# Performance work log

Hardware: AMD Instinct MI355X
Metric: run time of the kernel (lower is better)

Reference implementation:

```python
import jax, jax.numpy as jnp
import numpy as np

N_EMBD = 1024
N_HEAD = 16
HEAD_SIZE = N_EMBD // N_HEAD
EPS = 1e-5


def layernorm(x, g, b):
    mu = jnp.mean(x, axis=-1, keepdims=True)
    var = jnp.var(x, axis=-1, keepdims=True)
    return (x - mu) * jax.lax.rsqrt(var + EPS) * g + b


def setup_inputs() -> dict:
    key = jax.random.key(0)
    ks = jax.random.split(key, 12)
    s = 0.02
    C = N_EMBD
    return {
        "x": jax.random.normal(ks[0], (2, 2048, C), dtype=jnp.float32),
        "Wq": jax.random.normal(ks[1], (C, C), dtype=jnp.float32) * s,
        "Wk": jax.random.normal(ks[2], (C, C), dtype=jnp.float32) * s,
        "Wv": jax.random.normal(ks[3], (C, C), dtype=jnp.float32) * s,
        "Wo": jax.random.normal(ks[4], (C, C), dtype=jnp.float32) * s,
        "bo": jnp.zeros((C,), dtype=jnp.float32),
        "W1": jax.random.normal(ks[5], (C, 4 * C), dtype=jnp.float32) * s,
        "b1": jnp.zeros((4 * C,), dtype=jnp.float32),
        "W2": jax.random.normal(ks[6], (4 * C, C), dtype=jnp.float32) * s,
        "b2": jnp.zeros((C,), dtype=jnp.float32),
        "ln1_g": jnp.ones((C,), dtype=jnp.float32),
        "ln1_b": jnp.zeros((C,), dtype=jnp.float32),
        "ln2_g": jnp.ones((C,), dtype=jnp.float32),
        "ln2_b": jnp.zeros((C,), dtype=jnp.float32),
    }


def reference(x, Wq, Wk, Wv, Wo, bo, W1, b1, W2, b2, ln1_g, ln1_b, ln2_g, ln2_b):
    B, T, C = x.shape
    H, Dh = N_HEAD, HEAD_SIZE

    # --- self-attention branch ---
    h = layernorm(x, ln1_g, ln1_b)
    q = (h @ Wq).reshape(B, T, H, Dh)
    k = (h @ Wk).reshape(B, T, H, Dh)
    v = (h @ Wv).reshape(B, T, H, Dh)

    # NOTE: original scales by C**-0.5 (n_embd), not head_size**-0.5
    scale = C ** (-0.5)
    scores = jnp.einsum("bqhd,bkhd->bhqk", q, k) * scale  # [B,H,T,T]
    causal = jnp.tril(jnp.ones((T, T), dtype=bool))
    scores = jnp.where(causal, scores, -jnp.inf)
    wei = jax.nn.softmax(scores, axis=-1)
    attn = jnp.einsum("bhqk,bkhd->bqhd", wei, v).reshape(B, T, C)
    x = x + attn @ Wo + bo

    # --- MLP branch ---
    h2 = layernorm(x, ln2_g, ln2_b)
    ff = jax.nn.relu(h2 @ W1 + b1) @ W2 + b2
    return x + ff
```

## Files before the change

### kernel.cpp

```cpp
#include <hip/hip_runtime.h>

typedef unsigned short u16;
typedef __bf16 bf16;
typedef bf16 bf16x8 __attribute__((ext_vector_type(8)));
typedef float f32x4 __attribute__((ext_vector_type(4)));


__device__ __forceinline__ u16 f2bf(float f) {
  bf16 b = (bf16)f;
  return __builtin_bit_cast(u16, b);
}

__device__ __forceinline__ void gll16(void* lds, const void* g) {
  __builtin_amdgcn_global_load_lds((__attribute__((address_space(1))) void*)g,
                                   (__attribute__((address_space(3))) void*)lds,
                                   16, 0, 0);
}

__device__ __forceinline__ f32x4 mfma16(bf16x8 a, bf16x8 b, f32x4 c) {
  return __builtin_amdgcn_mfma_f32_16x16x32_bf16(a, b, c, 0, 0, 0);
}



__global__ __launch_bounds__(256)
void transpose_all(const float* __restrict__ Wq, const float* __restrict__ Wk,
                   const float* __restrict__ Wv, const float* __restrict__ Wo,
                   const float* __restrict__ W1, const float* __restrict__ W2,
                   u16* __restrict__ WqT, u16* __restrict__ WkT,
                   u16* __restrict__ WvT, u16* __restrict__ WoT,
                   u16* __restrict__ W1T, u16* __restrict__ W2T) {
  __shared__ float tile[32][33];
  const int id = blockIdx.x;
  const float* src;
  u16* dst;
  int R, C, t;
  if (id < 4096) {
    const int w = id >> 10;
    t = id & 1023; R = 1024; C = 1024;
    src = w == 0 ? Wq : w == 1 ? Wk : w == 2 ? Wv : Wo;
    dst = w == 0 ? WqT : w == 1 ? WkT : w == 2 ? WvT : WoT;
  } else if (id < 8192) {
    t = id - 4096; R = 1024; C = 4096; src = W1; dst = W1T;
  } else {
    t = id - 8192; R = 4096; C = 1024; src = W2; dst = W2T;
  }
  const int tilesx = C >> 5;
  const int c0 = (t % tilesx) * 32, r0 = (t / tilesx) * 32;
  const int tx = threadIdx.x, ty = threadIdx.y;
#pragma unroll
  for (int i = 0; i < 4; ++i)
    tile[ty + i * 8][tx] = src[(size_t)(r0 + ty + i * 8) * C + c0 + tx];
  __syncthreads();
#pragma unroll
  for (int i = 0; i < 4; ++i)
    dst[(size_t)(c0 + ty + i * 8) * R + r0 + tx] = f2bf(tile[tx][ty + i * 8]);
}


__global__ __launch_bounds__(256)
void ln_kernel(const float* __restrict__ x, const float* __restrict__ g,
               const float* __restrict__ bb, u16* __restrict__ h) {
  const int row = blockIdx.x;
  const int tid = threadIdx.x;
  const float4 xv = ((const float4*)(x + (size_t)row * 1024))[tid];
  float s = xv.x + xv.y + xv.z + xv.w;
  float q = xv.x * xv.x + xv.y * xv.y + xv.z * xv.z + xv.w * xv.w;
#pragma unroll
  for (int m = 1; m < 64; m <<= 1) {
    s += __shfl_xor(s, m);
    q += __shfl_xor(q, m);
  }
  __shared__ float ss[4], qq[4];
  const int wid = tid >> 6, lane = tid & 63;
  if (lane == 0) { ss[wid] = s; qq[wid] = q; }
  __syncthreads();
  s = ss[0] + ss[1] + ss[2] + ss[3];
  q = qq[0] + qq[1] + qq[2] + qq[3];
  const float mean = s * (1.0f / 1024.0f);
  const float var = q * (1.0f / 1024.0f) - mean * mean;
  const float rs = rsqrtf(var + 1e-5f);
  const float4 gv = ((const float4*)g)[tid];
  const float4 bv = ((const float4*)bb)[tid];
  ushort4 o;
  o.x = f2bf((xv.x - mean) * rs * gv.x + bv.x);
  o.y = f2bf((xv.y - mean) * rs * gv.y + bv.y);
  o.z = f2bf((xv.z - mean) * rs * gv.z + bv.z);
  o.w = f2bf((xv.w - mean) * rs * gv.w + bv.w);
  ((ushort4*)(h + (size_t)row * 1024))[tid] = o;
}


__device__ __forceinline__ void xcd_swizzle(int& bx, int& by, int& bz) {
  const int gx = gridDim.x, gy = gridDim.y;
  const int nwg = gx * gy * (int)gridDim.z;
  int flat = (int)blockIdx.x + gx * ((int)blockIdx.y + gy * (int)blockIdx.z);
  flat = (flat & 7) * (nwg >> 3) + (flat >> 3);
  bx = flat % gx;
  const int rem = flat / gx;
  by = rem % gy;
  bz = rem / gy;
}


template <int EPI>
__global__ __launch_bounds__(256)
void gemm_bt(const u16* __restrict__ A, const u16* __restrict__ Bt,
             const float* __restrict__ bias,
             void* __restrict__ O0, void* __restrict__ O1, void* __restrict__ O2,
             int M, int N, int K) {
  __shared__ __align__(16) u16 Alds[3][128 * 32];
  __shared__ __align__(16) u16 Blds[3][128 * 32];
  const int tid = threadIdx.x;
  const int lane = tid & 63, wid = tid >> 6;
  const int rl = lane & 15, kg = lane >> 4;
  const int ksw = (rl >> 1) & 3;
  int bx, by, bz;
  xcd_swizzle(bx, by, bz);
  const int m0 = by * 128, n0 = bx * 128;
  f32x4 acc[4][4];
#pragma unroll
  for (int i = 0; i < 4; ++i)
#pragma unroll
    for (int j = 0; j < 4; ++j) acc[i][j] = (f32x4){0.f, 0.f, 0.f, 0.f};
  const int wr = wid >> 1, wc = wid & 1;
  const int c0 = wid * 2, c1 = wid * 2 + 1;
  const int srow0 = c0 * 16 + (lane >> 2);
  const int srow1 = c1 * 16 + (lane >> 2);
  const int skol = (((lane & 3) ^ ((lane >> 3) & 3))) * 8;

#define STAGE_BT(buf, k0)                                                      \
  {                                                                            \
    gll16(Alds[buf] + c0 * 512, A + (size_t)(m0 + srow0) * K + (k0) + skol);   \
    gll16(Alds[buf] + c1 * 512, A + (size_t)(m0 + srow1) * K + (k0) + skol);   \
    gll16(Blds[buf] + c0 * 512, Bt + (size_t)(n0 + srow0) * K + (k0) + skol);  \
    gll16(Blds[buf] + c1 * 512, Bt + (size_t)(n0 + srow1) * K + (k0) + skol);  \
  }

  const int nt = K >> 5;
  STAGE_BT(0, 0);
  STAGE_BT(1, 32);
  int cur = 0;
  for (int t = 0; t < nt; ++t) {
    if (t + 1 < nt)
      asm volatile("s_waitcnt vmcnt(4)" ::: "memory");
    else
      asm volatile("s_waitcnt vmcnt(0)" ::: "memory");
    __builtin_amdgcn_s_barrier();
    if (t + 2 < nt) {
      const int nxt = cur >= 1 ? cur - 1 : cur + 2;
      STAGE_BT(nxt, (t + 2) << 5);
    }
    bf16x8 af[4], bfr[4];
#pragma unroll
    for (int m = 0; m < 4; ++m)
      af[m] = *(const bf16x8*)(Alds[cur] + (wr * 64 + m * 16 + rl) * 32 +
                               (kg ^ ksw) * 8);
#pragma unroll
    for (int n = 0; n < 4; ++n)
      bfr[n] = *(const bf16x8*)(Blds[cur] + (wc * 64 + n * 16 + rl) * 32 +
                                (kg ^ ksw) * 8);
    __builtin_amdgcn_s_setprio(1);
#pragma unroll
    for (int m = 0; m < 4; ++m)
#pragma unroll
      for (int n = 0; n < 4; ++n)
        acc[m][n] = mfma16(af[m], bfr[n], acc[m][n]);
    __builtin_amdgcn_s_setprio(0);
    cur = cur + 1 == 3 ? 0 : cur + 1;
  }
#undef STAGE_BT

#pragma unroll
  for (int m = 0; m < 4; ++m) {
#pragma unroll
    for (int n = 0; n < 4; ++n) {
      const int col = n0 + wc * 64 + n * 16 + rl;
      const int row0 = m0 + wr * 64 + m * 16 + kg * 4;
      if (EPI == 0) {
        const int seg = col >> 10;
        const int lc = col & 1023;
        if (seg == 2) {
          u16* vt = (u16*)O2;
          const size_t off =
              ((size_t)((row0 >> 11) * 16 + (lc >> 6)) * 64 + (lc & 63)) * 2048 +
              (row0 & 2047);
          ushort4 pk = {f2bf(acc[m][n][0]), f2bf(acc[m][n][1]),
                        f2bf(acc[m][n][2]), f2bf(acc[m][n][3])};
          *(ushort4*)(vt + off) = pk;
        } else {
          u16* o = (u16*)(seg == 0 ? O0 : O1);
#pragma unroll
          for (int r = 0; r < 4; ++r)
            o[(size_t)(row0 + r) * 1024 + lc] = f2bf(acc[m][n][r]);
        }
      } else {
        const float bv = bias[col];
#pragma unroll
        for (int r = 0; r < 4; ++r) {
          float v = acc[m][n][r] + bv;
          v = v > 0.f ? v : 0.f;
          ((u16*)O0)[(size_t)(row0 + r) * N + col] = f2bf(v);
        }
      }
    }
  }
}


__global__ __launch_bounds__(256)
void gemm64(const u16* __restrict__ A, const u16* __restrict__ Bt,
            const float* __restrict__ bias, const float* __restrict__ res,
            float* __restrict__ O, int M, int N, int K) {
  __shared__ __align__(16) u16 Alds[4][64 * 32];
  __shared__ __align__(16) u16 Blds[4][128 * 32];
  const int tid = threadIdx.x;
  const int lane = tid & 63, wid = tid >> 6;
  const int rl = lane & 15, kg = lane >> 4;
  const int ksw = (rl >> 1) & 3;
  int bx, by, bz;
  xcd_swizzle(bx, by, bz);
  const int m0 = by * 64, n0 = bx * 128;
  f32x4 acc[2][4];
#pragma unroll
  for (int i = 0; i < 2; ++i)
#pragma unroll
    for (int j = 0; j < 4; ++j) acc[i][j] = (f32x4){0.f, 0.f, 0.f, 0.f};
  const int wr = wid >> 1, wc = wid & 1;
  const int srow = lane >> 2;
  const int skol = (((lane & 3) ^ ((lane >> 3) & 3))) * 8;
  const int arow = wid * 16 + srow;
  const int brow0 = wid * 32 + srow;
  const int brow1 = wid * 32 + 16 + srow;

#define STAGE_64(buf, k0)                                                      \
  {                                                                            \
    gll16(Alds[buf] + wid * 512, A + (size_t)(m0 + arow) * K + (k0) + skol);   \
    gll16(Blds[buf] + wid * 1024,                                              \
          Bt + (size_t)(n0 + brow0) * K + (k0) + skol);                        \
    gll16(Blds[buf] + wid * 1024 + 512,                                        \
          Bt + (size_t)(n0 + brow1) * K + (k0) + skol);                        \
  }

  const int nt = K >> 5;
  STAGE_64(0, 0);
  STAGE_64(1, 32);
  STAGE_64(2, 64);
  for (int t = 0; t < nt; ++t) {
    const int cur = t & 3;
    if (t + 2 < nt)
      asm volatile("s_waitcnt vmcnt(6)" ::: "memory");
    else if (t + 1 < nt)
      asm volatile("s_waitcnt vmcnt(3)" ::: "memory");
    else
      asm volatile("s_waitcnt vmcnt(0)" ::: "memory");
    __builtin_amdgcn_s_barrier();
    if (t + 3 < nt) STAGE_64((t + 3) & 3, (t + 3) << 5);
    bf16x8 af[2], bfr[4];
#pragma unroll
    for (int m = 0; m < 2; ++m)
      af[m] = *(const bf16x8*)(Alds[cur] + (wr * 32 + m * 16 + rl) * 32 +
                               (kg ^ ksw) * 8);
#pragma unroll
    for (int n = 0; n < 4; ++n)
      bfr[n] = *(const bf16x8*)(Blds[cur] + (wc * 64 + n * 16 + rl) * 32 +
                                (kg ^ ksw) * 8);
    __builtin_amdgcn_s_setprio(1);
#pragma unroll
    for (int m = 0; m < 2; ++m)
#pragma unroll
      for (int n = 0; n < 4; ++n)
        acc[m][n] = mfma16(af[m], bfr[n], acc[m][n]);
    __builtin_amdgcn_s_setprio(0);
  }
#undef STAGE_64

#pragma unroll
  for (int m = 0; m < 2; ++m) {
#pragma unroll
    for (int n = 0; n < 4; ++n) {
      const int col = n0 + wc * 64 + n * 16 + rl;
      const int row0 = m0 + wr * 32 + m * 16 + kg * 4;
      const float bv = bias[col];
#pragma unroll
      for (int r = 0; r < 4; ++r) {
        const int row = row0 + r;
        O[(size_t)row * N + col] =
            acc[m][n][r] + bv + res[(size_t)row * N + col];
      }
    }
  }
}


#define SC2 0.045084220027780106f

__device__ __forceinline__ void attn_range(
    const u16* __restrict__ qg, const u16* __restrict__ kgl,
    const u16* __restrict__ vtb, size_t rowb, int cb, char* plw,
    int rl, int kg, int q0, int kvb, int kve, bool mask_last,
    f32x4 (&ot)[2][4], float (&lrun)[2]) {
  if (kvb >= kve) return;
  const int swz = (rl & 7) << 4;
  bf16x8 qf[2][2];
#pragma unroll
  for (int m = 0; m < 2; ++m) {
    const u16* qp = qg + (rowb + q0 + m * 16 + rl) * 1024 + cb + kg * 8;
    qf[m][0] = *(const bf16x8*)(qp);
    qf[m][1] = *(const bf16x8*)(qp + 32);
  }

  bf16x8 ka[4][2], kb[4][2];
#define LOADK(dst, kvi)                                                        \
  {                                                                            \
    const u16* krow = kgl + (rowb + (kvi) * 64 + rl) * 1024 + cb + kg * 8;     \
    _Pragma("unroll") for (int n = 0; n < 4; ++n) {                            \
      dst[n][0] = *(const bf16x8*)(krow + (size_t)n * 16 * 1024);              \
      dst[n][1] = *(const bf16x8*)(krow + (size_t)n * 16 * 1024 + 32);         \
    }                                                                          \
  }

#define BODY(kf, kvi)                                                          \
  {                                                                            \
    const int kv0 = (kvi) * 64;                                                \
    const u16* vrow = vtb + (size_t)rl * 2048 + kv0 + kg * 8;                  \
    bf16x8 vfr[4][2];                                                          \
    _Pragma("unroll") for (int dt = 0; dt < 4; ++dt) {                         \
      vfr[dt][0] = *(const bf16x8*)(vrow + (size_t)dt * 16 * 2048);            \
      vfr[dt][1] = *(const bf16x8*)(vrow + (size_t)dt * 16 * 2048 + 32);       \
    }                                                                          \
    const bool domask = mask_last && ((kvi) == kve - 1);                       \
    _Pragma("unroll") for (int m = 0; m < 2; ++m) {                            \
      f32x4 s[4];                                                              \
      __builtin_amdgcn_s_setprio(1);                                           \
      _Pragma("unroll") for (int n = 0; n < 4; ++n) {                          \
        f32x4 t = (f32x4){0.f, 0.f, 0.f, 0.f};                                 \
        t = mfma16(kf[n][0], qf[m][0], t);                                     \
        t = mfma16(kf[n][1], qf[m][1], t);                                     \
        s[n] = t;                                                              \
      }                                                                        \
      __builtin_amdgcn_s_setprio(0);                                           \
      if (domask) {                                                            \
        const int qrow = q0 + m * 16 + rl;                                     \
        _Pragma("unroll") for (int n = 0; n < 4; ++n)                          \
            _Pragma("unroll") for (int r = 0; r < 4; ++r) {                    \
          const int tk = kv0 + n * 16 + 4 * kg + r;                            \
          s[n][r] = (tk > qrow) ? -3e38f : s[n][r];                            \
        }                                                                      \
      }                                                                        \
      float ps = 0.f;                                                          \
      _Pragma("unroll") for (int n = 0; n < 4; ++n) {                          \
        const float p0 = exp2f(__builtin_fmaf(s[n][0], SC2, -8.f));            \
        const float p1 = exp2f(__builtin_fmaf(s[n][1], SC2, -8.f));            \
        const float p2 = exp2f(__builtin_fmaf(s[n][2], SC2, -8.f));            \
        const float p3 = exp2f(__builtin_fmaf(s[n][3], SC2, -8.f));            \
        ps += (p0 + p1) + (p2 + p3);                                           \
        ushort4 pk = {f2bf(p0), f2bf(p1), f2bf(p2), f2bf(p3)};                 \
        *(ushort4*)(plw + m * 2048 + ((rl * 128 + n * 32 + kg * 8) ^ swz)) =   \
            pk;                                                                \
      }                                                                        \
      lrun[m] += ps;                                                           \
    }                                                                          \
    _Pragma("unroll") for (int m = 0; m < 2; ++m) {                            \
      const bf16x8 pf0 =                                                       \
          *(const bf16x8*)(plw + m * 2048 + ((rl * 128 + kg * 16) ^ swz));     \
      const bf16x8 pf1 = *(const bf16x8*)(plw + m * 2048 +                     \
                                          ((rl * 128 + 64 + kg * 16) ^ swz));  \
      __builtin_amdgcn_s_setprio(1);                                           \
      _Pragma("unroll") for (int dt = 0; dt < 4; ++dt) {                       \
        ot[m][dt] = mfma16(vfr[dt][0], pf0, ot[m][dt]);                        \
        ot[m][dt] = mfma16(vfr[dt][1], pf1, ot[m][dt]);                        \
      }                                                                        \
      __builtin_amdgcn_s_setprio(0);                                           \
    }                                                                          \
  }

  LOADK(ka, kvb);
  int kv = kvb;
  for (;;) {
    if (kv + 1 < kve) LOADK(kb, kv + 1);
    BODY(ka, kv);
    ++kv;
    if (kv >= kve) break;
    if (kv + 1 < kve) LOADK(ka, kv + 1);
    BODY(kb, kv);
    ++kv;
    if (kv >= kve) break;
  }
#undef LOADK
#undef BODY
}

__global__ __launch_bounds__(128)
void attn_kernel(const u16* __restrict__ qg, const u16* __restrict__ kgl,
                 const u16* __restrict__ vtg, u16* __restrict__ og) {
  const int tid = threadIdx.x, lane = tid & 63, wid = tid >> 6;
  const int rl = lane & 15, kg = lane >> 4;
  const int flat = blockIdx.x;
  const int bh = (flat & 7) * 4 + ((flat >> 3) & 3);
  const int pr = flat >> 5;
  const int jA = pr, jB = 63 - pr;
  const int nA = (jA >> 1) + 1, nB = (jB >> 1) + 1;
  const int a = (nB - nA) >> 1;
  const size_t rowb = (size_t)(bh >> 4) * 2048;
  const int cb = (bh & 15) * 64;
  const u16* vtb = vtg + (size_t)bh * 64 * 2048;

  __shared__ __align__(16) char Pl[2][4096];
  __shared__ __align__(16) float MrgO[2][4][64][4];
  __shared__ float MrgL[2][16];
  char* plw = Pl[wid];

  f32x4 ot[2][4];
  float lrun[2] = {0.f, 0.f};
#pragma unroll
  for (int m = 0; m < 2; ++m)
#pragma unroll
    for (int dt = 0; dt < 4; ++dt) ot[m][dt] = (f32x4){0.f, 0.f, 0.f, 0.f};

  if (wid == 0) {
    attn_range(qg, kgl, vtb, rowb, cb, plw, rl, kg, jA * 32, 0, nA, true,
               ot, lrun);
#pragma unroll
    for (int m = 0; m < 2; ++m) {
      lrun[m] += __shfl_xor(lrun[m], 16);
      lrun[m] += __shfl_xor(lrun[m], 32);
      const float inv = 1.f / lrun[m];
      u16* orow = og + (rowb + jA * 32 + m * 16 + rl) * 1024 + cb;
#pragma unroll
      for (int dt = 0; dt < 4; ++dt) {
        ushort4 ok = {f2bf(ot[m][dt][0] * inv), f2bf(ot[m][dt][1] * inv),
                      f2bf(ot[m][dt][2] * inv), f2bf(ot[m][dt][3] * inv)};
        *(ushort4*)(orow + dt * 16 + 4 * kg) = ok;
      }
      lrun[m] = 0.f;
#pragma unroll
      for (int dt = 0; dt < 4; ++dt) ot[m][dt] = (f32x4){0.f, 0.f, 0.f, 0.f};
    }
    attn_range(qg, kgl, vtb, rowb, cb, plw, rl, kg, jB * 32, 0, a, false,
               ot, lrun);
  } else {
    attn_range(qg, kgl, vtb, rowb, cb, plw, rl, kg, jB * 32, a, nB, true,
               ot, lrun);
#pragma unroll
    for (int m = 0; m < 2; ++m) {
      lrun[m] += __shfl_xor(lrun[m], 16);
      lrun[m] += __shfl_xor(lrun[m], 32);
#pragma unroll
      for (int dt = 0; dt < 4; ++dt)
        *(f32x4*)(&MrgO[m][dt][lane][0]) = ot[m][dt];
      if (kg == 0) MrgL[m][rl] = lrun[m];
    }
  }
  __syncthreads();
  if (wid == 0) {
#pragma unroll
    for (int m = 0; m < 2; ++m) {
      lrun[m] += __shfl_xor(lrun[m], 16);
      lrun[m] += __shfl_xor(lrun[m], 32);
      const float inv = 1.f / (lrun[m] + MrgL[m][rl]);
      u16* orow = og + (rowb + jB * 32 + m * 16 + rl) * 1024 + cb;
#pragma unroll
      for (int dt = 0; dt < 4; ++dt) {
        const f32x4 o1 = *(const f32x4*)(&MrgO[m][dt][lane][0]);
        ushort4 ok;
#pragma unroll
        for (int r = 0; r < 4; ++r)
          ((u16*)&ok)[r] = f2bf((ot[m][dt][r] + o1[r]) * inv);
        *(ushort4*)(orow + dt * 16 + 4 * kg) = ok;
      }
    }
  }
}


extern "C" void kernel_launch(void* const* d_in, const int* in_sizes, int n_in,
                              void* d_out, int out_size, void* d_ws, size_t ws_size,
                              hipStream_t stream) {
  const float* x    = (const float*)d_in[0];
  const float* Wq   = (const float*)d_in[1];
  const float* Wk   = (const float*)d_in[2];
  const float* Wv   = (const float*)d_in[3];
  const float* Wo   = (const float*)d_in[4];
  const float* bo   = (const float*)d_in[5];
  const float* W1   = (const float*)d_in[6];
  const float* b1   = (const float*)d_in[7];
  const float* W2   = (const float*)d_in[8];
  const float* b2   = (const float*)d_in[9];
  const float* ln1g = (const float*)d_in[10];
  const float* ln1b = (const float*)d_in[11];
  const float* ln2g = (const float*)d_in[12];
  const float* ln2b = (const float*)d_in[13];
  float* out = (float*)d_out;

  char* ws = (char*)d_ws;
  const size_t MB = 1024 * 1024;
  u16* WqT  = (u16*)(ws + 0 * MB);
  u16* WoT  = (u16*)(ws + 6 * MB);
  u16* W1T  = (u16*)(ws + 8 * MB);
  u16* W2T  = (u16*)(ws + 16 * MB);
  u16* h    = (u16*)(ws + 24 * MB);
  u16* q    = (u16*)(ws + 32 * MB);
  u16* k    = (u16*)(ws + 40 * MB);
  u16* vt   = (u16*)(ws + 48 * MB);
  u16* attn = (u16*)(ws + 56 * MB);
  float* x1 = (float*)(ws + 64 * MB);
  u16* ff1  = (u16*)(ws + 32 * MB);
  u16* WkT  = WqT + 1024 * 1024;
  u16* WvT  = WqT + 2 * 1024 * 1024;

  dim3 tblk(32, 8);
  transpose_all<<<12288, tblk, 0, stream>>>(Wq, Wk, Wv, Wo, W1, W2,
                                            WqT, WkT, WvT, WoT, W1T, W2T);

  ln_kernel<<<4096, 256, 0, stream>>>(x, ln1g, ln1b, h);

  gemm_bt<0><<<dim3(24, 32), 256, 0, stream>>>(h, WqT, nullptr,
                                               q, k, vt, 4096, 3072, 1024);

  attn_kernel<<<1024, 128, 0, stream>>>(q, k, vt, attn);

  gemm64<<<dim3(8, 64), 256, 0, stream>>>(attn, WoT, bo, x, x1,
                                          4096, 1024, 1024);

  ln_kernel<<<4096, 256, 0, stream>>>(x1, ln2g, ln2b, h);

  gemm_bt<1><<<dim3(32, 32), 256, 0, stream>>>(h, W1T, b1, ff1, ff1, ff1,
                                               4096, 4096, 1024);

  gemm64<<<dim3(8, 64), 256, 0, stream>>>(ff1, W2T, b2, x1, out,
                                          4096, 1024, 4096);
}
```

Baseline: 269.7 us.

## Split attention KV range across four waves and widen gemm64 K-tile

The attention kernel now gives each block a single 32-row query tile and splits its causal KV range across four waves, merging the partial outputs and row sums through shared memory. This replaces the paired short/long tile balancing between two waves, doubling the block count for more parallelism. Separately, gemm64 moves from a K-step of 32 with four LDS buffers to a K-step of 64 with three buffers and an XOR swizzle over eight 16-byte slots, halving barriers per K. The risks are extra LDS for the partial merge, which may lower occupancy, and three-stage rather than four-stage buffering in the GEMM.

```diff
diff --git a/kernel.cpp b/kernel.cpp
--- a/kernel.cpp
+++ b/kernel.cpp
@@ -20,7 +20,6 @@
 __device__ __forceinline__ f32x4 mfma16(bf16x8 a, bf16x8 b, f32x4 c) {
   return __builtin_amdgcn_mfma_f32_16x16x32_bf16(a, b, c, 0, 0, 0);
 }
-
 
 
 __global__ __launch_bounds__(256)
@@ -212,12 +211,11 @@
 void gemm64(const u16* __restrict__ A, const u16* __restrict__ Bt,
             const float* __restrict__ bias, const float* __restrict__ res,
             float* __restrict__ O, int M, int N, int K) {
-  __shared__ __align__(16) u16 Alds[4][64 * 32];
-  __shared__ __align__(16) u16 Blds[4][128 * 32];
+  __shared__ __align__(16) u16 Alds[3][64 * 64];
+  __shared__ __align__(16) u16 Blds[3][128 * 64];
   const int tid = threadIdx.x;
   const int lane = tid & 63, wid = tid >> 6;
   const int rl = lane & 15, kg = lane >> 4;
-  const int ksw = (rl >> 1) & 3;
   int bx, by, bz;
   xcd_swizzle(bx, by, bz);
   const int m0 = by * 64, n0 = bx * 128;
@@ -227,53 +225,71 @@
 #pragma unroll
     for (int j = 0; j < 4; ++j) acc[i][j] = (f32x4){0.f, 0.f, 0.f, 0.f};
   const int wr = wid >> 1, wc = wid & 1;
-  const int srow = lane >> 2;
-  const int skol = (((lane & 3) ^ ((lane >> 3) & 3))) * 8;
-  const int arow = wid * 16 + srow;
-  const int brow0 = wid * 32 + srow;
-  const int brow1 = wid * 32 + 16 + srow;
+  const int lrow = lane >> 3;
+  const int lslot = lane & 7;
+
+#define SRCA(base_r, k0)                                                       \
+  (A + (size_t)(m0 + (base_r) + lrow) * K + (k0) +                             \
+   ((lslot ^ (((base_r) + lrow) & 7)) * 8))
+#define SRCB(base_r, k0)                                                       \
+  (Bt + (size_t)(n0 + (base_r) + lrow) * K + (k0) +                            \
+   ((lslot ^ (((base_r) + lrow) & 7)) * 8))
 
 #define STAGE_64(buf, k0)                                                      \
   {                                                                            \
-    gll16(Alds[buf] + wid * 512, A + (size_t)(m0 + arow) * K + (k0) + skol);   \
-    gll16(Blds[buf] + wid * 1024,                                              \
-          Bt + (size_t)(n0 + brow0) * K + (k0) + skol);                        \
-    gll16(Blds[buf] + wid * 1024 + 512,                                        \
-          Bt + (size_t)(n0 + brow1) * K + (k0) + skol);                        \
-  }
-
-  const int nt = K >> 5;
+    gll16(Alds[buf] + (wid * 16 + 0) * 64, SRCA(wid * 16 + 0, k0));            \
+    gll16(Alds[buf] + (wid * 16 + 8) * 64, SRCA(wid * 16 + 8, k0));            \
+    gll16(Blds[buf] + (wid * 32 + 0) * 64, SRCB(wid * 32 + 0, k0));            \
+    gll16(Blds[buf] + (wid * 32 + 8) * 64, SRCB(wid * 32 + 8, k0));            \
+    gll16(Blds[buf] + (wid * 32 + 16) * 64, SRCB(wid * 32 + 16, k0));          \
+    gll16(Blds[buf] + (wid * 32 + 24) * 64, SRCB(wid * 32 + 24, k0));          \
+  }
+
+  const int nt = K >> 6;
   STAGE_64(0, 0);
-  STAGE_64(1, 32);
-  STAGE_64(2, 64);
+  STAGE_64(1, 64);
+  int cur = 0;
   for (int t = 0; t < nt; ++t) {
-    const int cur = t & 3;
-    if (t + 2 < nt)
+    if (t + 1 < nt)
       asm volatile("s_waitcnt vmcnt(6)" ::: "memory");
-    else if (t + 1 < nt)
-      asm volatile("s_waitcnt vmcnt(3)" ::: "memory");
     else
       asm volatile("s_waitcnt vmcnt(0)" ::: "memory");
     __builtin_amdgcn_s_barrier();
-    if (t + 3 < nt) STAGE_64((t + 3) & 3, (t + 3) << 5);
-    bf16x8 af[2], bfr[4];
+    if (t + 2 < nt) {
+      const int nxt = cur >= 1 ? cur - 1 : cur + 2;
+      STAGE_64(nxt, (t + 2) << 6);
+    }
+    bf16x8 af[2][2], bfr[4][2];
+#pragma unroll
+    for (int m = 0; m < 2; ++m) {
+      const int row = wr * 32 + m * 16 + rl;
+#pragma unroll
+      for (int kf = 0; kf < 2; ++kf)
+        af[m][kf] = *(const bf16x8*)(Alds[cur] + row * 64 +
+                                     ((kf * 4 + kg) ^ (row & 7)) * 8);
+    }
+#pragma unroll
+    for (int n = 0; n < 4; ++n) {
+      const int row = wc * 64 + n * 16 + rl;
+#pragma unroll
+      for (int kf = 0; kf < 2; ++kf)
+        bfr[n][kf] = *(const bf16x8*)(Blds[cur] + row * 64 +
+                                      ((kf * 4 + kg) ^ (row & 7)) * 8);
+    }
+    __builtin_amdgcn_s_setprio(1);
 #pragma unroll
     for (int m = 0; m < 2; ++m)
-      af[m] = *(const bf16x8*)(Alds[cur] + (wr * 32 + m * 16 + rl) * 32 +
-                               (kg ^ ksw) * 8);
-#pragma unroll
-    for (int n = 0; n < 4; ++n)
-      bfr[n] = *(const bf16x8*)(Blds[cur] + (wc * 64 + n * 16 + rl) * 32 +
-                                (kg ^ ksw) * 8);
-    __builtin_amdgcn_s_setprio(1);
-#pragma unroll
-    for (int m = 0; m < 2; ++m)
-#pragma unroll
-      for (int n = 0; n < 4; ++n)
-        acc[m][n] = mfma16(af[m], bfr[n], acc[m][n]);
+#pragma unroll
+      for (int n = 0; n < 4; ++n) {
+        acc[m][n] = mfma16(af[m][0], bfr[n][0], acc[m][n]);
+        acc[m][n] = mfma16(af[m][1], bfr[n][1], acc[m][n]);
+      }
     __builtin_amdgcn_s_setprio(0);
+    cur = cur + 1 == 3 ? 0 : cur + 1;
   }
 #undef STAGE_64
+#undef SRCA
+#undef SRCB
 
 #pragma unroll
   for (int m = 0; m < 2; ++m) {
@@ -391,25 +407,25 @@
 #undef BODY
 }
 
-__global__ __launch_bounds__(128)
+__global__ __launch_bounds__(256)
 void attn_kernel(const u16* __restrict__ qg, const u16* __restrict__ kgl,
                  const u16* __restrict__ vtg, u16* __restrict__ og) {
   const int tid = threadIdx.x, lane = tid & 63, wid = tid >> 6;
   const int rl = lane & 15, kg = lane >> 4;
   const int flat = blockIdx.x;
   const int bh = (flat & 7) * 4 + ((flat >> 3) & 3);
-  const int pr = flat >> 5;
-  const int jA = pr, jB = 63 - pr;
-  const int nA = (jA >> 1) + 1, nB = (jB >> 1) + 1;
-  const int a = (nB - nA) >> 1;
+  const int j = 63 - (flat >> 5);
+  const int q0 = j * 32;
+  const int nkv = (j >> 1) + 1;
+  const int kb = (nkv * wid) >> 2;
+  const int ke = (nkv * (wid + 1)) >> 2;
   const size_t rowb = (size_t)(bh >> 4) * 2048;
   const int cb = (bh & 15) * 64;
   const u16* vtb = vtg + (size_t)bh * 64 * 2048;
 
-  __shared__ __align__(16) char Pl[2][4096];
-  __shared__ __align__(16) float MrgO[2][4][64][4];
-  __shared__ float MrgL[2][16];
-  char* plw = Pl[wid];
+  __shared__ __align__(16) char Pl[4][4096];
+  __shared__ __align__(16) f32x4 PartO[4][2][4][64];
+  __shared__ float PartL[4][2][16];
 
   f32x4 ot[2][4];
   float lrun[2] = {0.f, 0.f};
@@ -418,57 +434,32 @@
 #pragma unroll
     for (int dt = 0; dt < 4; ++dt) ot[m][dt] = (f32x4){0.f, 0.f, 0.f, 0.f};
 
-  if (wid == 0) {
-    attn_range(qg, kgl, vtb, rowb, cb, plw, rl, kg, jA * 32, 0, nA, true,
-               ot, lrun);
-#pragma unroll
-    for (int m = 0; m < 2; ++m) {
-      lrun[m] += __shfl_xor(lrun[m], 16);
-      lrun[m] += __shfl_xor(lrun[m], 32);
-      const float inv = 1.f / lrun[m];
-      u16* orow = og + (rowb + jA * 32 + m * 16 + rl) * 1024 + cb;
-#pragma unroll
-      for (int dt = 0; dt < 4; ++dt) {
-        ushort4 ok = {f2bf(ot[m][dt][0] * inv), f2bf(ot[m][dt][1] * inv),
-                      f2bf(ot[m][dt][2] * inv), f2bf(ot[m][dt][3] * inv)};
-        *(ushort4*)(orow + dt * 16 + 4 * kg) = ok;
-      }
-      lrun[m] = 0.f;
-#pragma unroll
-      for (int dt = 0; dt < 4; ++dt) ot[m][dt] = (f32x4){0.f, 0.f, 0.f, 0.f};
-    }
-    attn_range(qg, kgl, vtb, rowb, cb, plw, rl, kg, jB * 32, 0, a, false,
-               ot, lrun);
-  } else {
-    attn_range(qg, kgl, vtb, rowb, cb, plw, rl, kg, jB * 32, a, nB, true,
-               ot, lrun);
-#pragma unroll
-    for (int m = 0; m < 2; ++m) {
-      lrun[m] += __shfl_xor(lrun[m], 16);
-      lrun[m] += __shfl_xor(lrun[m], 32);
-#pragma unroll
-      for (int dt = 0; dt < 4; ++dt)
-        *(f32x4*)(&MrgO[m][dt][lane][0]) = ot[m][dt];
-      if (kg == 0) MrgL[m][rl] = lrun[m];
-    }
+  attn_range(qg, kgl, vtb, rowb, cb, Pl[wid], rl, kg, q0, kb, ke,
+             wid == 3, ot, lrun);
+
+#pragma unroll
+  for (int m = 0; m < 2; ++m) {
+    lrun[m] += __shfl_xor(lrun[m], 16);
+    lrun[m] += __shfl_xor(lrun[m], 32);
+#pragma unroll
+    for (int dt = 0; dt < 4; ++dt) PartO[wid][m][dt][lane] = ot[m][dt];
+    if (kg == 0) PartL[wid][m][rl] = lrun[m];
   }
   __syncthreads();
-  if (wid == 0) {
-#pragma unroll
-    for (int m = 0; m < 2; ++m) {
-      lrun[m] += __shfl_xor(lrun[m], 16);
-      lrun[m] += __shfl_xor(lrun[m], 32);
-      const float inv = 1.f / (lrun[m] + MrgL[m][rl]);
-      u16* orow = og + (rowb + jB * 32 + m * 16 + rl) * 1024 + cb;
-#pragma unroll
-      for (int dt = 0; dt < 4; ++dt) {
-        const f32x4 o1 = *(const f32x4*)(&MrgO[m][dt][lane][0]);
-        ushort4 ok;
-#pragma unroll
-        for (int r = 0; r < 4; ++r)
-          ((u16*)&ok)[r] = f2bf((ot[m][dt][r] + o1[r]) * inv);
-        *(ushort4*)(orow + dt * 16 + 4 * kg) = ok;
-      }
+
+  if (wid < 2) {
+    const int m = wid;
+    const float l = PartL[0][m][rl] + PartL[1][m][rl] +
+                    PartL[2][m][rl] + PartL[3][m][rl];
+    const float inv = 1.f / l;
+    u16* orow = og + (rowb + q0 + m * 16 + rl) * 1024 + cb;
+#pragma unroll
+    for (int dt = 0; dt < 4; ++dt) {
+      const f32x4 o = PartO[0][m][dt][lane] + PartO[1][m][dt][lane] +
+                      PartO[2][m][dt][lane] + PartO[3][m][dt][lane];
+      ushort4 ok = {f2bf(o[0] * inv), f2bf(o[1] * inv),
+                    f2bf(o[2] * inv), f2bf(o[3] * inv)};
+      *(ushort4*)(orow + dt * 16 + 4 * kg) = ok;
     }
   }
 }
@@ -518,7 +509,7 @@
   gemm_bt<0><<<dim3(24, 32), 256, 0, stream>>>(h, WqT, nullptr,
                                                q, k, vt, 4096, 3072, 1024);
 
-  attn_kernel<<<1024, 128, 0, stream>>>(q, k, vt, attn);
+  attn_kernel<<<2048, 256, 0, stream>>>(q, k, vt, attn);
 
   gemm64<<<dim3(8, 64), 256, 0, stream>>>(attn, WoT, bo, x, x1,
                                           4096, 1024, 1024);
```

New measurement: 273.0 us. Within noise of the previous version (+1.2%).
